# Performance work log

Measured on AMD Instinct MI355X. Metric: run time of the kernel, lower is better.

## Reference

```python
import jax, jax.numpy as jnp
import numpy as np

N_NODES = 50000
N_EDGES = 800000
N_GRAPHS = 64


def setup_inputs() -> dict:
    key = jax.random.key(0)
    ks = jax.random.split(key, 12)

    def w(k, shape):
        fan_in = shape[0]
        return jax.random.normal(k, shape, dtype=jnp.float32) / np.sqrt(fan_in)

    x = jax.random.normal(ks[0], (N_NODES, 6), dtype=jnp.float32)
    edge_index = jax.random.randint(ks[1], (2, N_EDGES), 0, N_NODES, dtype=jnp.int64)
    batch = jnp.sort(jax.random.randint(ks[2], (N_NODES,), 0, N_GRAPHS, dtype=jnp.int64))
    return {
        "x": x,
        "edge_index": edge_index,
        "batch": batch,
        "W_in": w(ks[3], (6, 64)),
        "b_in": jnp.zeros((64,), jnp.float32),
        "W1": w(ks[4], (64, 128)),
        "b1": jnp.zeros((128,), jnp.float32),
        "W2": w(ks[5], (128, 128)),
        "b2": jnp.zeros((128,), jnp.float32),
        "Wp": w(ks[6], (256, 256)),
        "bp": jnp.zeros((256,), jnp.float32),
    }


def reference(x, edge_index, batch, W_in, b_in, W1, b1, W2, b2, Wp, bp):
    n = x.shape[0]
    self_loop = jnp.arange(n, dtype=edge_index.dtype)
    src = jnp.concatenate([edge_index[0], self_loop])  # [E+N]
    dst = jnp.concatenate([edge_index[1], self_loop])
    # GCN symmetric normalization with self-loops (PyG GCNConv default)
    deg = jax.ops.segment_sum(jnp.ones_like(dst, x.dtype), dst, num_segments=n)
    dinv = jax.lax.rsqrt(deg)  # deg >= 1 because of self-loops
    norm = (dinv[src] * dinv[dst])[:, None]  # [E+N, 1]

    def gcn(h, W, b):
        hw = h @ W                       # linear first, like GCNConv
        msg = hw[src] * norm             # gather + normalize per edge
        return jax.ops.segment_sum(msg, dst, num_segments=n) + b

    h = x @ W_in + b_in                  # input_projection
    h = jax.nn.relu(gcn(h, W1, b1))      # relu(gnn1(...))
    h = jax.nn.relu(gcn(h, W2, b2))      # relu(gnn2(...))

    # global mean / max pooling over batch segments
    counts = jax.ops.segment_sum(jnp.ones((n,), h.dtype), batch, num_segments=N_GRAPHS)
    h_mean = jax.ops.segment_sum(h, batch, num_segments=N_GRAPHS) / jnp.maximum(counts, 1.0)[:, None]
    h_max = jax.ops.segment_max(h, batch, num_segments=N_GRAPHS)
    h_max = jnp.where(counts[:, None] > 0, h_max, 0.0)
    h_graph = jnp.concatenate([h_mean, h_max], axis=1)  # [G, 256]

    # projection MLP: Linear + ReLU (Dropout is identity in eval)
    return jax.nn.relu(h_graph @ Wp + bp)
```

## Files before the change

kernel.cpp:

```cpp
#include <hip/hip_runtime.h>
#include <hip/hip_fp16.h>

#define N_NODES 50000
#define N_EDGES 800000
#define N_GRAPHS 64
#define N_PAD 50048

#define CB 256
#define EPB (N_EDGES / CB)
#define NBUCKET ((N_NODES + 255) / 256)

typedef _Float16 f16x8 __attribute__((ext_vector_type(8)));
typedef float f32x4 __attribute__((ext_vector_type(4)));

struct H8 { __half2 a, b, c, d; };


__global__ void k_prep(const float* __restrict__ W_in, const float* __restrict__ b_in,
                       const float* __restrict__ W1, const float* __restrict__ W2,
                       _Float16* __restrict__ Wt2, float* __restrict__ Wcz,
                       float* psum, float* pmax, int* totals) {
    int idx = blockIdx.x * blockDim.x + threadIdx.x;
    if (idx < 128 * 128) {
        int n = idx >> 7, k = idx & 127;
        Wt2[idx] = (_Float16)W2[k * 128 + n];
    } else if (idx < 128 * 128 + 1024) {
        int j = idx - 128 * 128;
        int ch = j >> 3, k = j & 7;
        float acc = 0.f;
        if (k < 6) {
            for (int q = 0; q < 64; q++) acc += W_in[k * 64 + q] * W1[q * 128 + ch];
        } else if (k == 6) {
            for (int q = 0; q < 64; q++) acc += b_in[q] * W1[q * 128 + ch];
        }
        Wcz[k * 128 + ch] = acc;
    }
    if (idx < N_GRAPHS * 128) { psum[idx] = 0.f; pmax[idx] = 0.f; }
    if (idx < 256) totals[idx] = 0;
}


__global__ __launch_bounds__(256) void k_coarse_hist(const int* __restrict__ dst,
                                                     int* __restrict__ totals) {
    __shared__ int hist[NBUCKET];
    int t = threadIdx.x, b = blockIdx.x;
    for (int i = t; i < NBUCKET; i += 256) hist[i] = 0;
    __syncthreads();
    int e0 = b * EPB;
    for (int e = e0 + t; e < e0 + EPB; e += 256)
        atomicAdd(&hist[dst[e] >> 8], 1);
    __syncthreads();
    for (int i = t; i < NBUCKET; i += 256)
        if (hist[i] > 0) atomicAdd(&totals[i], hist[i]);
}

__global__ void k_bucket_scan(const int* __restrict__ totals, int* __restrict__ bucket_base,
                              int* __restrict__ gcursor, const int* __restrict__ batch,
                              float* __restrict__ pcnt) {
    __shared__ int sh[256];
    int t = threadIdx.x;
    int v = (t < NBUCKET) ? totals[t] : 0;
    sh[t] = v;
    __syncthreads();
    for (int off = 1; off < 256; off <<= 1) {
        int u = (t >= off) ? sh[t - off] : 0;
        __syncthreads();
        sh[t] += u;
        __syncthreads();
    }
    if (t < NBUCKET) {
        int base = sh[t] - v;
        bucket_base[t] = base;
        gcursor[t] = base;
    }
    if (t == 0) bucket_base[NBUCKET] = N_EDGES;
    if (t <= N_GRAPHS) {
        int lo = 0, hi = N_NODES;
        while (lo < hi) {
            int mid = (lo + hi) >> 1;
            if (batch[mid] < t) lo = mid + 1; else hi = mid;
        }
        sh[t] = lo;
    }
    __syncthreads();
    if (t < N_GRAPHS) pcnt[t] = (float)(sh[t + 1] - sh[t]);
}

__global__ __launch_bounds__(256) void k_coarse_scatter(
        const int* __restrict__ src, const int* __restrict__ dst,
        int* __restrict__ gcursor, unsigned int* __restrict__ esort) {
    __shared__ int cur[NBUCKET];
    int t = threadIdx.x, b = blockIdx.x;
    for (int i = t; i < NBUCKET; i += 256) cur[i] = 0;
    __syncthreads();
    int e0 = b * EPB;
    for (int e = e0 + t; e < e0 + EPB; e += 256)
        atomicAdd(&cur[dst[e] >> 8], 1);
    __syncthreads();
    for (int i = t; i < NBUCKET; i += 256) {
        int cnt = cur[i];
        cur[i] = (cnt > 0) ? atomicAdd(&gcursor[i], cnt) : 0;
    }
    __syncthreads();
    for (int e = e0 + t; e < e0 + EPB; e += 256) {
        int d = dst[e];
        int slot = atomicAdd(&cur[d >> 8], 1);
        esort[slot] = ((unsigned)(d & 255) << 16) | (unsigned)src[e];
    }
}

__global__ __launch_bounds__(256) void k_fine_fill_p(
        const unsigned int* __restrict__ esort, const int* __restrict__ bucket_base,
        int* __restrict__ col, int* __restrict__ row_ptr, float* __restrict__ dinv,
        const float* __restrict__ x, float* __restrict__ p) {
    __shared__ int hist[256];
    __shared__ int sc[256];
    __shared__ int cur[256];
    int t = threadIdx.x, b = blockIdx.x;
    hist[t] = 0;
    __syncthreads();
    int base = bucket_base[b], end = bucket_base[b + 1];
    for (int e = base + t; e < end; e += 256)
        atomicAdd(&hist[(esort[e] >> 16) & 255], 1);
    __syncthreads();
    int v = hist[t];
    sc[t] = v;
    __syncthreads();
    for (int off = 1; off < 256; off <<= 1) {
        int u = (t >= off) ? sc[t - off] : 0;
        __syncthreads();
        sc[t] += u;
        __syncthreads();
    }
    int start = base + sc[t] - v;
    cur[t] = start;
    int node = b * 256 + t;
    float di = rsqrtf((float)(v + 1));
    if (node < N_NODES) {
        row_ptr[node] = start;
        dinv[node] = di;
        float pr[8];
#pragma unroll
        for (int k = 0; k < 6; k++) pr[k] = x[node * 6 + k] * di;
        pr[6] = di;
        pr[7] = 0.f;
        *(f32x4*)&p[(size_t)node * 8] = *(f32x4*)&pr[0];
        *(f32x4*)&p[(size_t)node * 8 + 4] = *(f32x4*)&pr[4];
    }
    if (b == 0 && t == 0) row_ptr[N_NODES] = N_EDGES;
    __syncthreads();
    for (int e = base + t; e < end; e += 256) {
        unsigned pk = esort[e];
        int slot = atomicAdd(&cur[(pk >> 16) & 255], 1);
        col[slot] = (int)(pk & 0xffffu);
    }
}

__global__ __launch_bounds__(256, 8) void k_agg_proj(
        const float* __restrict__ p, const int* __restrict__ row_ptr,
        const int* __restrict__ col, const float* __restrict__ Wcz,
        const float* __restrict__ b1, const float* __restrict__ dinv,
        _Float16* __restrict__ g1, int n) {
    __shared__ float tl[32][8];
    __shared__ float Wl[8 * 128];
    __shared__ float bl[128];
    int t = threadIdx.x;
    for (int i = t; i < 1024; i += 256) Wl[i] = Wcz[i];
    if (t < 128) bl[t] = b1[t];

    int rg = t >> 3, ck = t & 7;
    int row = blockIdx.x * 32 + rg;
    float acc = 0.f;
    if (row < n) {
        acc = p[(size_t)row * 8 + ck];
        int e = row_ptr[row], e1 = row_ptr[row + 1];
        for (; e + 3 < e1; e += 4) {
            int c0 = col[e], c1 = col[e + 1], c2 = col[e + 2], c3 = col[e + 3];
            float v0 = p[(size_t)c0 * 8 + ck];
            float v1 = p[(size_t)c1 * 8 + ck];
            float v2 = p[(size_t)c2 * 8 + ck];
            float v3 = p[(size_t)c3 * 8 + ck];
            acc += (v0 + v1) + (v2 + v3);
        }
        for (; e < e1; e++) acc += p[(size_t)col[e] * 8 + ck];
    }
    tl[rg][ck] = acc;
    __syncthreads();

    int rg2 = t >> 3, oc = t & 7;
    int row2 = blockIdx.x * 32 + rg2;
    if (row2 < n) {
        float tr[7];
#pragma unroll
        for (int k = 0; k < 7; k++) tr[k] = tl[rg2][k];
        float di = dinv[row2];
        f16x8 o0, o1;
#pragma unroll
        for (int c = 0; c < 16; c++) {
            int ch = oc * 16 + c;
            float z = 0.f;
#pragma unroll
            for (int k = 0; k < 7; k++) z += tr[k] * Wl[k * 128 + ch];
            z = di * z + bl[ch];
            float h = fmaxf(z, 0.f) * di;
            if (c < 8) o0[c] = (_Float16)h; else o1[c - 8] = (_Float16)h;
        }
        *(f16x8*)&g1[(size_t)row2 * 128 + oc * 16] = o0;
        *(f16x8*)&g1[(size_t)row2 * 128 + oc * 16 + 8] = o1;
    }
}

template <int K, int ROWS, bool HALF_OUT, bool POOL>
__global__ __launch_bounds__(256, 8) void k_gnn(
        const _Float16* __restrict__ g, const int* __restrict__ row_ptr,
        const int* __restrict__ col, const _Float16* __restrict__ Wt_h,
        const float* __restrict__ b, const float* __restrict__ dinv,
        void* __restrict__ outp, const int* __restrict__ batch,
        float* __restrict__ psum, float* __restrict__ pmax, int n) {
    constexpr int KP = K + 8;
    constexpr int TPR = 256 / ROWS;
    constexpr int CO8 = K / 8;
    static_assert(K / TPR == 8, "8 channels per gather thread");
    constexpr int S_BYTES = ROWS * KP * 2;
    constexpr int H_BYTES = POOL ? ROWS * 128 * 4 : 0;
    constexpr int SMEM = S_BYTES > H_BYTES ? S_BYTES : H_BYTES;
    __shared__ __align__(16) char smem[SMEM];
    _Float16* Sl = (_Float16*)smem;
    float* Hs = (float*)smem;
    int t = threadIdx.x;

    {
        int row_local = t / TPR;
        int ck = t % TPR;
        int row = blockIdx.x * ROWS + row_local;
        float accA[8] = {};
        float accB[8] = {};
        const H8* gb = (const H8*)g;
        auto addv = [](float* acc, H8 v) {
            float2 f;
            f = __half22float2(v.a); acc[0] += f.x; acc[1] += f.y;
            f = __half22float2(v.b); acc[2] += f.x; acc[3] += f.y;
            f = __half22float2(v.c); acc[4] += f.x; acc[5] += f.y;
            f = __half22float2(v.d); acc[6] += f.x; acc[7] += f.y;
        };
        if (row < n) {
            addv(accA, gb[(size_t)row * CO8 + ck]);
            int e = row_ptr[row], e1 = row_ptr[row + 1];
            for (; e + 3 < e1; e += 4) {
                int c0 = col[e], c1 = col[e + 1], c2 = col[e + 2], c3 = col[e + 3];
                H8 v0 = gb[(size_t)c0 * CO8 + ck];
                H8 v1 = gb[(size_t)c1 * CO8 + ck];
                H8 v2 = gb[(size_t)c2 * CO8 + ck];
                H8 v3 = gb[(size_t)c3 * CO8 + ck];
                addv(accA, v0);
                addv(accB, v1);
                addv(accA, v2);
                addv(accB, v3);
            }
            if (e + 1 < e1) {
                H8 v0 = gb[(size_t)col[e] * CO8 + ck];
                H8 v1 = gb[(size_t)col[e + 1] * CO8 + ck];
                addv(accA, v0);
                addv(accB, v1);
                e += 2;
            }
            if (e < e1) addv(accA, gb[(size_t)col[e] * CO8 + ck]);
        }
        f16x8 o;
#pragma unroll
        for (int q = 0; q < 8; q++) o[q] = (_Float16)(accA[q] + accB[q]);
        *(f16x8*)&Sl[row_local * KP + ck * 8] = o;
    }
    __syncthreads();

    int wave = t >> 6;
    int lane = t & 63;
    int m = lane & 15;
    int quad = lane >> 4;
    constexpr int COLT = (ROWS == 16) ? 2 : 4;
    int col_base = (ROWS == 16) ? wave * 32 : (wave >> 1) * 64;
    int rbl = (ROWS == 16) ? 0 : (wave & 1) * 16;
    int wrow0 = blockIdx.x * ROWS + rbl;

    f32x4 acc[COLT] = {};
#pragma unroll
    for (int k0 = 0; k0 < K; k0 += 32) {
        f16x8 a = *(const f16x8*)&Sl[(rbl + m) * KP + k0 + quad * 8];
#pragma unroll
        for (int ct = 0; ct < COLT; ct++) {
            f16x8 bw = *(const f16x8*)(Wt_h + (size_t)(col_base + ct * 16 + m) * K + k0 + quad * 8);
            acc[ct] = __builtin_amdgcn_mfma_f32_16x16x32_f16(a, bw, acc[ct], 0, 0, 0);
        }
    }

    if (!POOL) {
#pragma unroll
        for (int r = 0; r < 4; r++) {
            int row = wrow0 + quad * 4 + r;
            if (row < n) {
                float di = dinv[row];
#pragma unroll
                for (int ct = 0; ct < COLT; ct++) {
                    int colb = col_base + ct * 16 + m;
                    float v = fmaxf(di * acc[ct][r] + b[colb], 0.f);
                    if (HALF_OUT)
                        ((_Float16*)outp)[(size_t)row * 128 + colb] = (_Float16)(v * di);
                    else
                        ((float*)outp)[(size_t)row * 128 + colb] = v;
                }
            }
        }
    } else {
        __syncthreads();
#pragma unroll
        for (int r = 0; r < 4; r++) {
            int rl = quad * 4 + r;
            int row = wrow0 + rl;
            float di = (row < n) ? dinv[row] : 0.f;
#pragma unroll
            for (int ct = 0; ct < COLT; ct++) {
                int colb = col_base + ct * 16 + m;
                float v = fmaxf(di * acc[ct][r] + b[colb], 0.f);
                Hs[rl * 128 + colb] = (row < n) ? v : 0.f;
            }
        }
        __syncthreads();
        if (t < 128) {
            int colb = t;
            int row0b = blockIdx.x * ROWS;
            float s = 0.f, mx = 0.f;
            int gcur = batch[row0b < n ? row0b : (n - 1)];
            for (int rl = 0; rl < ROWS; rl++) {
                int row = row0b + rl;
                if (row >= n) break;
                int gi = batch[row];
                if (gi != gcur) {
                    atomicAdd(&psum[gcur * 128 + colb], s);
                    atomicMax((int*)&pmax[gcur * 128 + colb], __float_as_int(mx));
                    s = 0.f; mx = 0.f; gcur = gi;
                }
                float v = Hs[rl * 128 + colb];
                s += v;
                mx = fmaxf(mx, v);
            }
            atomicAdd(&psum[gcur * 128 + colb], s);
            atomicMax((int*)&pmax[gcur * 128 + colb], __float_as_int(mx));
        }
    }
}


__global__ void k_final(const float* __restrict__ psum, const float* __restrict__ pmax,
                        const float* __restrict__ pcnt, const float* __restrict__ Wp,
                        const float* __restrict__ bp, float* __restrict__ out) {
    int t = blockIdx.x * blockDim.x + threadIdx.x;
    if (t >= N_GRAPHS * 256) return;
    int g = t >> 8, j = t & 255;
    float inv = 1.0f / fmaxf(pcnt[g], 1.0f);
    float acc = bp[j];
#pragma unroll 4
    for (int k = 0; k < 128; k++) acc += (psum[g * 128 + k] * inv) * Wp[k * 256 + j];
#pragma unroll 4
    for (int k = 0; k < 128; k++) acc += pmax[g * 128 + k] * Wp[(128 + k) * 256 + j];
    out[t] = fmaxf(acc, 0.f);
}

extern "C" void kernel_launch(void* const* d_in, const int* in_sizes, int n_in,
                              void* d_out, int out_size, void* d_ws, size_t ws_size,
                              hipStream_t stream) {
    const int N = N_NODES, E = N_EDGES;
    const float* x    = (const float*)d_in[0];
    const int*   ei   = (const int*)d_in[1];
    const int*   src  = ei;
    const int*   dst  = ei + E;
    const int*   batch= (const int*)d_in[2];
    const float* W_in = (const float*)d_in[3];
    const float* b_in = (const float*)d_in[4];
    const float* W1   = (const float*)d_in[5];
    const float* b1   = (const float*)d_in[6];
    const float* W2   = (const float*)d_in[7];
    const float* b2   = (const float*)d_in[8];
    const float* Wp   = (const float*)d_in[9];
    const float* bp   = (const float*)d_in[10];
    float* out = (float*)d_out;

    char* p8 = (char*)d_ws;
    int* totals      = (int*)p8;   p8 += 256 * 4;
    int* bucket_base = (int*)p8;   p8 += 256 * 4;
    int* gcursor     = (int*)p8;   p8 += 256 * 4;
    int* row_ptr     = (int*)p8;   p8 += (N_PAD + 64) * 4;
    int* col         = (int*)p8;   p8 += (size_t)N_EDGES * 4;
    unsigned* esort  = (unsigned*)p8; p8 += (size_t)N_EDGES * 4;
    float* dinv      = (float*)p8; p8 += N_PAD * 4;
    float* Wcz       = (float*)p8; p8 += 1024 * 4;
    _Float16* Wt2    = (_Float16*)p8; p8 += 128 * 128 * 2;
    float* pfeat     = (float*)p8; p8 += (size_t)N_PAD * 8 * 4;
    _Float16* g1h    = (_Float16*)p8; p8 += (size_t)N_PAD * 128 * 2;
    float* psum      = (float*)p8; p8 += N_GRAPHS * 128 * 4;
    float* pmax      = (float*)p8; p8 += N_GRAPHS * 128 * 4;
    float* pcnt      = (float*)p8;

    const int TB = 256;
    dim3 blk(TB);

    k_prep<<<(128 * 128 + 1024 + TB - 1) / TB, blk, 0, stream>>>(
        W_in, b_in, W1, W2, Wt2, Wcz, psum, pmax, totals);

    k_coarse_hist<<<CB, blk, 0, stream>>>(dst, totals);
    k_bucket_scan<<<1, blk, 0, stream>>>(totals, bucket_base, gcursor, batch, pcnt);
    k_coarse_scatter<<<CB, blk, 0, stream>>>(src, dst, gcursor, esort);
    k_fine_fill_p<<<NBUCKET, blk, 0, stream>>>(esort, bucket_base, col, row_ptr, dinv,
                                               x, pfeat);

    k_agg_proj<<<(N + 31) / 32, blk, 0, stream>>>(pfeat, row_ptr, col, Wcz, b1, dinv,
                                                  g1h, N);

    k_gnn<128, 16, false, true><<<(N + 15) / 16, blk, 0, stream>>>(
        g1h, row_ptr, col, Wt2, b2, dinv, nullptr, batch, psum, pmax, N);

    k_final<<<(N_GRAPHS * 256 + TB - 1) / TB, blk, 0, stream>>>(psum, pmax, pcnt, Wp, bp, out);
}
```

Baseline: 201.4 us.

## Store layer-1 features in channel-quarter planes and gather per quarter with interleaved MFMA

The layer-1 output is now written as four 32-channel planes, each laid out over all padded nodes, instead of one 128-channel row per node. The layer-2 kernel gathers one quarter at a time, with 16 threads per row loading half2 each, then does that quarter's MFMA slice before moving on. Each plane is 3.2 MB instead of 12.8 MB for the whole array, so the aim is to keep the gathered working set cache-resident. The cost is re-reading the CSR column indices four times, smaller 4-byte gather loads, and extra block barriers.

After: 232.2 us. +15.2%, slower.

```diff
diff --git a/kernel.cpp b/kernel.cpp
--- a/kernel.cpp
+++ b/kernel.cpp
@@ -12,8 +12,6 @@
 
 typedef _Float16 f16x8 __attribute__((ext_vector_type(8)));
 typedef float f32x4 __attribute__((ext_vector_type(4)));
-
-struct H8 { __half2 a, b, c, d; };
 
 
 __global__ void k_prep(const float* __restrict__ W_in, const float* __restrict__ b_in,
@@ -205,147 +203,110 @@
             float h = fmaxf(z, 0.f) * di;
             if (c < 8) o0[c] = (_Float16)h; else o1[c - 8] = (_Float16)h;
         }
-        *(f16x8*)&g1[(size_t)row2 * 128 + oc * 16] = o0;
-        *(f16x8*)&g1[(size_t)row2 * 128 + oc * 16 + 8] = o1;
-    }
-}
-
-template <int K, int ROWS, bool HALF_OUT, bool POOL>
-__global__ __launch_bounds__(256, 8) void k_gnn(
+        size_t base = ((size_t)(oc >> 1) * N_PAD + row2) * 32 + (oc & 1) * 16;
+        *(f16x8*)&g1[base] = o0;
+        *(f16x8*)&g1[base + 8] = o1;
+    }
+}
+
+__global__ __launch_bounds__(256, 8) void k_gnn2q(
         const _Float16* __restrict__ g, const int* __restrict__ row_ptr,
         const int* __restrict__ col, const _Float16* __restrict__ Wt_h,
         const float* __restrict__ b, const float* __restrict__ dinv,
-        void* __restrict__ outp, const int* __restrict__ batch,
-        float* __restrict__ psum, float* __restrict__ pmax, int n) {
-    constexpr int KP = K + 8;
-    constexpr int TPR = 256 / ROWS;
-    constexpr int CO8 = K / 8;
-    static_assert(K / TPR == 8, "8 channels per gather thread");
-    constexpr int S_BYTES = ROWS * KP * 2;
-    constexpr int H_BYTES = POOL ? ROWS * 128 * 4 : 0;
-    constexpr int SMEM = S_BYTES > H_BYTES ? S_BYTES : H_BYTES;
-    __shared__ __align__(16) char smem[SMEM];
+        const int* __restrict__ batch, float* __restrict__ psum,
+        float* __restrict__ pmax, int n) {
+    constexpr int ROWS = 16;
+    constexpr int KP = 40;
+    __shared__ __align__(16) char smem[ROWS * 128 * 4];
     _Float16* Sl = (_Float16*)smem;
     float* Hs = (float*)smem;
     int t = threadIdx.x;
 
-    {
-        int row_local = t / TPR;
-        int ck = t % TPR;
-        int row = blockIdx.x * ROWS + row_local;
-        float accA[8] = {};
-        float accB[8] = {};
-        const H8* gb = (const H8*)g;
-        auto addv = [](float* acc, H8 v) {
-            float2 f;
-            f = __half22float2(v.a); acc[0] += f.x; acc[1] += f.y;
-            f = __half22float2(v.b); acc[2] += f.x; acc[3] += f.y;
-            f = __half22float2(v.c); acc[4] += f.x; acc[5] += f.y;
-            f = __half22float2(v.d); acc[6] += f.x; acc[7] += f.y;
-        };
-        if (row < n) {
-            addv(accA, gb[(size_t)row * CO8 + ck]);
-            int e = row_ptr[row], e1 = row_ptr[row + 1];
-            for (; e + 3 < e1; e += 4) {
-                int c0 = col[e], c1 = col[e + 1], c2 = col[e + 2], c3 = col[e + 3];
-                H8 v0 = gb[(size_t)c0 * CO8 + ck];
-                H8 v1 = gb[(size_t)c1 * CO8 + ck];
-                H8 v2 = gb[(size_t)c2 * CO8 + ck];
-                H8 v3 = gb[(size_t)c3 * CO8 + ck];
-                addv(accA, v0);
-                addv(accB, v1);
-                addv(accA, v2);
-                addv(accB, v3);
-            }
-            if (e + 1 < e1) {
-                H8 v0 = gb[(size_t)col[e] * CO8 + ck];
-                H8 v1 = gb[(size_t)col[e + 1] * CO8 + ck];
-                addv(accA, v0);
-                addv(accB, v1);
-                e += 2;
-            }
-            if (e < e1) addv(accA, gb[(size_t)col[e] * CO8 + ck]);
-        }
-        f16x8 o;
-#pragma unroll
-        for (int q = 0; q < 8; q++) o[q] = (_Float16)(accA[q] + accB[q]);
-        *(f16x8*)&Sl[row_local * KP + ck * 8] = o;
-    }
-    __syncthreads();
+    int rl = t >> 4, ck = t & 15;
+    int row = blockIdx.x * ROWS + rl;
+    int e0 = 0, e1 = 0;
+    if (row < n) { e0 = row_ptr[row]; e1 = row_ptr[row + 1]; }
 
     int wave = t >> 6;
     int lane = t & 63;
     int m = lane & 15;
     int quad = lane >> 4;
-    constexpr int COLT = (ROWS == 16) ? 2 : 4;
-    int col_base = (ROWS == 16) ? wave * 32 : (wave >> 1) * 64;
-    int rbl = (ROWS == 16) ? 0 : (wave & 1) * 16;
-    int wrow0 = blockIdx.x * ROWS + rbl;
-
-    f32x4 acc[COLT] = {};
-#pragma unroll
-    for (int k0 = 0; k0 < K; k0 += 32) {
-        f16x8 a = *(const f16x8*)&Sl[(rbl + m) * KP + k0 + quad * 8];
-#pragma unroll
-        for (int ct = 0; ct < COLT; ct++) {
-            f16x8 bw = *(const f16x8*)(Wt_h + (size_t)(col_base + ct * 16 + m) * K + k0 + quad * 8);
+    int col_base = wave * 32;
+
+    f32x4 acc[2] = {};
+
+#pragma unroll
+    for (int q = 0; q < 4; q++) {
+        const __half2* gq = (const __half2*)(g + (size_t)q * (N_PAD * 32));
+        float a0 = 0.f, a1 = 0.f, b0 = 0.f, b1 = 0.f;
+        if (row < n) {
+            __half2 sv = gq[(size_t)row * 16 + ck];
+            float2 f = __half22float2(sv);
+            a0 += f.x; a1 += f.y;
+            int e = e0;
+            for (; e + 3 < e1; e += 4) {
+                int c0 = col[e], c1 = col[e + 1], c2 = col[e + 2], c3 = col[e + 3];
+                __half2 v0 = gq[(size_t)c0 * 16 + ck];
+                __half2 v1 = gq[(size_t)c1 * 16 + ck];
+                __half2 v2 = gq[(size_t)c2 * 16 + ck];
+                __half2 v3 = gq[(size_t)c3 * 16 + ck];
+                float2 f0 = __half22float2(v0), f1 = __half22float2(v1);
+                float2 f2 = __half22float2(v2), f3 = __half22float2(v3);
+                a0 += f0.x; a1 += f0.y; b0 += f1.x; b1 += f1.y;
+                a0 += f2.x; a1 += f2.y; b0 += f3.x; b1 += f3.y;
+            }
+            for (; e < e1; e++) {
+                __half2 v = gq[(size_t)col[e] * 16 + ck];
+                float2 f = __half22float2(v);
+                a0 += f.x; a1 += f.y;
+            }
+        }
+        *(__half2*)&Sl[rl * KP + ck * 2] = __floats2half2_rn(a0 + b0, a1 + b1);
+        __syncthreads();
+
+        f16x8 a = *(const f16x8*)&Sl[m * KP + quad * 8];
+#pragma unroll
+        for (int ct = 0; ct < 2; ct++) {
+            f16x8 bw = *(const f16x8*)(Wt_h + (size_t)(col_base + ct * 16 + m) * 128
+                                       + q * 32 + quad * 8);
             acc[ct] = __builtin_amdgcn_mfma_f32_16x16x32_f16(a, bw, acc[ct], 0, 0, 0);
         }
-    }
-
-    if (!POOL) {
-#pragma unroll
-        for (int r = 0; r < 4; r++) {
-            int row = wrow0 + quad * 4 + r;
-            if (row < n) {
-                float di = dinv[row];
-#pragma unroll
-                for (int ct = 0; ct < COLT; ct++) {
-                    int colb = col_base + ct * 16 + m;
-                    float v = fmaxf(di * acc[ct][r] + b[colb], 0.f);
-                    if (HALF_OUT)
-                        ((_Float16*)outp)[(size_t)row * 128 + colb] = (_Float16)(v * di);
-                    else
-                        ((float*)outp)[(size_t)row * 128 + colb] = v;
-                }
+        __syncthreads();
+    }
+
+#pragma unroll
+    for (int r = 0; r < 4; r++) {
+        int rll = quad * 4 + r;
+        int rw = blockIdx.x * ROWS + rll;
+        float di = (rw < n) ? dinv[rw] : 0.f;
+#pragma unroll
+        for (int ct = 0; ct < 2; ct++) {
+            int colb = col_base + ct * 16 + m;
+            float v = fmaxf(di * acc[ct][r] + b[colb], 0.f);
+            Hs[rll * 128 + colb] = (rw < n) ? v : 0.f;
+        }
+    }
+    __syncthreads();
+    if (t < 128) {
+        int colb = t;
+        int row0b = blockIdx.x * ROWS;
+        float s = 0.f, mx = 0.f;
+        int gcur = batch[row0b < n ? row0b : (n - 1)];
+        for (int rr = 0; rr < ROWS; rr++) {
+            int rw = row0b + rr;
+            if (rw >= n) break;
+            int gi = batch[rw];
+            if (gi != gcur) {
+                atomicAdd(&psum[gcur * 128 + colb], s);
+                atomicMax((int*)&pmax[gcur * 128 + colb], __float_as_int(mx));
+                s = 0.f; mx = 0.f; gcur = gi;
             }
-        }
-    } else {
-        __syncthreads();
-#pragma unroll
-        for (int r = 0; r < 4; r++) {
-            int rl = quad * 4 + r;
-            int row = wrow0 + rl;
-            float di = (row < n) ? dinv[row] : 0.f;
-#pragma unroll
-            for (int ct = 0; ct < COLT; ct++) {
-                int colb = col_base + ct * 16 + m;
-                float v = fmaxf(di * acc[ct][r] + b[colb], 0.f);
-                Hs[rl * 128 + colb] = (row < n) ? v : 0.f;
-            }
-        }
-        __syncthreads();
-        if (t < 128) {
-            int colb = t;
-            int row0b = blockIdx.x * ROWS;
-            float s = 0.f, mx = 0.f;
-            int gcur = batch[row0b < n ? row0b : (n - 1)];
-            for (int rl = 0; rl < ROWS; rl++) {
-                int row = row0b + rl;
-                if (row >= n) break;
-                int gi = batch[row];
-                if (gi != gcur) {
-                    atomicAdd(&psum[gcur * 128 + colb], s);
-                    atomicMax((int*)&pmax[gcur * 128 + colb], __float_as_int(mx));
-                    s = 0.f; mx = 0.f; gcur = gi;
-                }
-                float v = Hs[rl * 128 + colb];
-                s += v;
-                mx = fmaxf(mx, v);
-            }
-            atomicAdd(&psum[gcur * 128 + colb], s);
-            atomicMax((int*)&pmax[gcur * 128 + colb], __float_as_int(mx));
-        }
+            float v = Hs[rr * 128 + colb];
+            s += v;
+            mx = fmaxf(mx, v);
+        }
+        atomicAdd(&psum[gcur * 128 + colb], s);
+        atomicMax((int*)&pmax[gcur * 128 + colb], __float_as_int(mx));
     }
 }
 
@@ -415,8 +376,8 @@
     k_agg_proj<<<(N + 31) / 32, blk, 0, stream>>>(pfeat, row_ptr, col, Wcz, b1, dinv,
                                                   g1h, N);
 
-    k_gnn<128, 16, false, true><<<(N + 15) / 16, blk, 0, stream>>>(
-        g1h, row_ptr, col, Wt2, b2, dinv, nullptr, batch, psum, pmax, N);
+    k_gnn2q<<<(N + 15) / 16, blk, 0, stream>>>(
+        g1h, row_ptr, col, Wt2, b2, dinv, batch, psum, pmax, N);
 
     k_final<<<(N_GRAPHS * 256 + TB - 1) / TB, blk, 0, stream>>>(psum, pmax, pcnt, Wp, bp, out);
 }
```
